# Kernel tuning notes

Measured on AMD Instinct MI355X. Metric: run time of the kernel, lower is better.

## Reference

```python
import jax, jax.numpy as jnp
import numpy as np

NUM_CLASSES = 10
OUT_DIM = 16
NUM_ROUTING = 3
ROUTING_BIAS = 0.1


def _squash(s):
    # s: [B, C, D]; norm over last (out_capsule) dim, matches torch norm(dim=2)
    norm = jnp.linalg.norm(s, axis=2, keepdims=True)
    # s / (1+norm^2) / norm * norm^2 == s * norm / (1 + norm^2)
    return s * norm / (1.0 + norm * norm)


def setup_inputs() -> dict:
    key = jax.random.key(0)
    k1, k2 = jax.random.split(key)
    B, N, IN_DIM = 256, 2304, 8
    x = jax.random.normal(k1, (B, N, IN_DIM), dtype=jnp.float32)
    # kaiming-normal-ish init for W [N, in_dim, classes*out_dim]
    W = jax.random.normal(k2, (N, IN_DIM, NUM_CLASSES * OUT_DIM), dtype=jnp.float32) * np.sqrt(2.0 / IN_DIM)
    return {"x": x, "W": W}


def reference(x, W):
    B, N, _ = x.shape
    # broadcast-multiply+sum in original == per-capsule matmul
    u_hat = jnp.einsum('bni,nio->bno', x, W).reshape(B, N, NUM_CLASSES, OUT_DIM)
    u_hat_sg = jax.lax.stop_gradient(u_hat)
    b = jnp.zeros((B, N, NUM_CLASSES), dtype=x.dtype)
    v = None
    for i in range(NUM_ROUTING):
        c = jax.nn.softmax(b, axis=2)  # [B, N, C]
        if i == NUM_ROUTING - 1:
            s = jnp.einsum('bnc,bncd->bcd', c, u_hat) + ROUTING_BIAS
            v = _squash(s)
        else:
            s = jnp.einsum('bnc,bncd->bcd', c, u_hat_sg) + ROUTING_BIAS
            # NOTE: original updates b with pre-squash s (not v) -- kept faithful
            b = b + jnp.einsum('bncd,bcd->bnc', u_hat_sg, s)
    return v
```

## Files before the change

### kernel.cpp

```cpp
#include <hip/hip_runtime.h>
#include <math.h>

#define B_TOT   256
#define N_TOT   2304
#define IN_DIM  8
#define NC      10
#define OD      16
#define CD      160
#define RBIAS   0.1f

#define BTILE    64
#define NS       192
#define NPB      (N_TOT / NS)
#define NTHREADS 640
#define XR       (NPB * IN_DIM + 4)
#define LB       72
#define NF4      (B_TOT * CD / 4)
#define RCOLS    32
#define RGRPS    8
#define RYPER    (NS / RGRPS)

template <int FIRST>
__global__ __launch_bounds__(NTHREADS) void routing_round(
    const float* __restrict__ x,
    const float* __restrict__ W,
    const float* __restrict__ S_acc,
    float* __restrict__ part)
{
    __shared__ float sh_x[BTILE * XR];
    __shared__ float sh_lg[2][NC * LB];

    const int tid = threadIdx.x;
    const int b0  = blockIdx.x * BTILE;
    const int n0  = blockIdx.y * NPB;
    const int b   = tid & 63;
    const int cu  = __builtin_amdgcn_readfirstlane(tid >> 6);

    {
        const int XT4 = BTILE * (NPB * IN_DIM / 4);
        for (int k = tid; k < XT4; k += NTHREADS) {
            int bb   = k / (NPB * 2);
            int off4 = k - bb * (NPB * 2);
            float4 v = *(const float4*)(x + ((size_t)(b0 + bb) * N_TOT + n0) * IN_DIM + off4 * 4);
            *(float4*)(&sh_x[bb * XR + off4 * 4]) = v;
        }
    }

    float S[OD];
    if (!FIRST) {
        const float4* sp = (const float4*)(S_acc + (size_t)(b0 + b) * CD + cu * OD);
        #pragma unroll
        for (int q = 0; q < 4; q++) ((float4*)S)[q] = sp[q];
    }

    float acc[OD];
    #pragma unroll
    for (int d = 0; d < OD; d++) acc[d] = 0.f;

    __syncthreads();

    const float* Wc = W + cu * OD;

    for (int nn = 0; nn < NPB; nn++) {
        float xf[IN_DIM];
        {
            const float4* xp = (const float4*)(&sh_x[b * XR + nn * IN_DIM]);
            ((float4*)xf)[0] = xp[0];
            ((float4*)xf)[1] = xp[1];
        }

        const float* Wn = Wc + (size_t)(n0 + nn) * (IN_DIM * CD);
        float u[OD];
        #pragma unroll
        for (int d = 0; d < OD; d++) u[d] = xf[0] * Wn[d];
        #pragma unroll
        for (int i = 1; i < IN_DIM; i++) {
            const float* Wi = Wn + i * CD;
            #pragma unroll
            for (int d = 0; d < OD; d++) u[d] = fmaf(xf[i], Wi[d], u[d]);
        }

        if (!FIRST) {
            const int cur = nn & 1;
            float lg = 0.f;
            #pragma unroll
            for (int d = 0; d < OD; d++) lg = fmaf(u[d], S[d], lg);
            sh_lg[cur][cu * LB + b] = lg;
            __syncthreads();

            float m = -1e30f;
            float row[NC];
            #pragma unroll
            for (int k = 0; k < NC; k++) {
                row[k] = sh_lg[cur][k * LB + b];
                m = fmaxf(m, row[k]);
            }
            float den = 0.f;
            #pragma unroll
            for (int k = 0; k < NC; k++) den += __expf(row[k] - m);
            float cw = __expf(lg - m) / den;

            #pragma unroll
            for (int d = 0; d < OD; d++) acc[d] = fmaf(cw, u[d], acc[d]);
        } else {
            #pragma unroll
            for (int d = 0; d < OD; d++) acc[d] += u[d];
        }
    }

    float* dst = part + ((size_t)blockIdx.y * B_TOT + (b0 + b)) * CD + cu * OD;
    #pragma unroll
    for (int q = 0; q < 4; q++)
        ((float4*)dst)[q] = ((float4*)acc)[q];
}

__global__ __launch_bounds__(256) void reduce_round(
    const float* __restrict__ part,
    float* __restrict__ S_acc,
    float* __restrict__ v_out,
    float scale, int round)
{
    __shared__ float4 sh[RGRPS][RCOLS];

    const int col = threadIdx.x & (RCOLS - 1);
    const int grp = threadIdx.x >> 5;
    const int g   = blockIdx.x * RCOLS + col;

    const float4* p4 = (const float4*)part + (size_t)grp * NF4 + g;
    float4 s = { 0.f, 0.f, 0.f, 0.f };
    #pragma unroll 4
    for (int y = 0; y < RYPER; y++) {
        float4 t = p4[(size_t)y * RGRPS * NF4];
        s.x += t.x; s.y += t.y; s.z += t.z; s.w += t.w;
    }
    sh[grp][col] = s;
    __syncthreads();

    if (threadIdx.x < RCOLS) {
        float4 t = { 0.f, 0.f, 0.f, 0.f };
        #pragma unroll
        for (int k = 0; k < RGRPS; k++) {
            float4 q = sh[k][col];
            t.x += q.x; t.y += q.y; t.z += q.z; t.w += q.w;
        }
        t.x = t.x * scale + RBIAS;
        t.y = t.y * scale + RBIAS;
        t.z = t.z * scale + RBIAS;
        t.w = t.w * scale + RBIAS;

        if (round == 0) {
            ((float4*)S_acc)[g] = t;
        } else if (round == 1) {
            float4 o = ((float4*)S_acc)[g];
            o.x += t.x; o.y += t.y; o.z += t.z; o.w += t.w;
            ((float4*)S_acc)[g] = o;
        } else {
            float ss = t.x * t.x + t.y * t.y + t.z * t.z + t.w * t.w;
            ss += __shfl_xor(ss, 1, 64);
            ss += __shfl_xor(ss, 2, 64);
            float norm = sqrtf(ss);
            float k2 = norm / (1.0f + ss);
            float4 v = { t.x * k2, t.y * k2, t.z * k2, t.w * k2 };
            ((float4*)v_out)[g] = v;
        }
    }
}

extern "C" void kernel_launch(void* const* d_in, const int* in_sizes, int n_in,
                              void* d_out, int out_size, void* d_ws, size_t ws_size,
                              hipStream_t stream) {
    const float* x = (const float*)d_in[0];
    const float* W = (const float*)d_in[1];
    float* out = (float*)d_out;

    float* part  = (float*)d_ws;
    float* S_acc = part + (size_t)NS * B_TOT * CD;

    const dim3 rgrid(B_TOT / BTILE, NS);
    const int  RG = NF4 / RCOLS;

    routing_round<1><<<rgrid, NTHREADS, 0, stream>>>(x, W, S_acc, part);
    reduce_round<<<RG, 256, 0, stream>>>(part, S_acc, out, 0.1f, 0);

    routing_round<0><<<rgrid, NTHREADS, 0, stream>>>(x, W, S_acc, part);
    reduce_round<<<RG, 256, 0, stream>>>(part, S_acc, out, 1.0f, 1);

    routing_round<0><<<rgrid, NTHREADS, 0, stream>>>(x, W, S_acc, part);
    reduce_round<<<RG, 256, 0, stream>>>(part, S_acc, out, 1.0f, 2);
}
```

Measured before the change: 214.2 us.

## Compute u_hat with split-bf16 MFMA and shuffle-based softmax routing

```diff
diff --git a/kernel.cpp b/kernel.cpp
--- a/kernel.cpp
+++ b/kernel.cpp
@@ -9,109 +9,135 @@
 #define CD      160
 #define RBIAS   0.1f
 
-#define BTILE    64
-#define NS       192
-#define NPB      (N_TOT / NS)
-#define NTHREADS 640
-#define XR       (NPB * IN_DIM + 4)
-#define LB       72
-#define NF4      (B_TOT * CD / 4)
-#define RCOLS    32
-#define RGRPS    8
-#define RYPER    (NS / RGRPS)
+#define NS      128
+#define NPB     (N_TOT / NS)
+#define WROW    (IN_DIM * CD)
+#define NF4     (B_TOT * CD / 4)
+#define NXCD    8
+
+typedef __attribute__((ext_vector_type(8))) short bf16x8;
+typedef __attribute__((ext_vector_type(4))) float f32x4;
+
+__device__ __forceinline__ unsigned int rne_hi(unsigned int b) {
+    return (b + 0x7FFFu + ((b >> 16) & 1u)) & 0xFFFF0000u;
+}
+__device__ __forceinline__ void split2(float f, unsigned int& h, unsigned int& l) {
+    unsigned int xb = __float_as_uint(f);
+    h = rne_hi(xb);
+    float fl = f - __uint_as_float(h);
+    l = __float_as_uint(fl) & 0xFFFF0000u;
+}
 
 template <int FIRST>
-__global__ __launch_bounds__(NTHREADS) void routing_round(
+__global__ __launch_bounds__(512) void routing_round(
     const float* __restrict__ x,
     const float* __restrict__ W,
     const float* __restrict__ S_acc,
     float* __restrict__ part)
 {
-    __shared__ float sh_x[BTILE * XR];
-    __shared__ float sh_lg[2][NC * LB];
-
-    const int tid = threadIdx.x;
-    const int b0  = blockIdx.x * BTILE;
-    const int n0  = blockIdx.y * NPB;
-    const int b   = tid & 63;
-    const int cu  = __builtin_amdgcn_readfirstlane(tid >> 6);
-
-    {
-        const int XT4 = BTILE * (NPB * IN_DIM / 4);
-        for (int k = tid; k < XT4; k += NTHREADS) {
-            int bb   = k / (NPB * 2);
-            int off4 = k - bb * (NPB * 2);
-            float4 v = *(const float4*)(x + ((size_t)(b0 + bb) * N_TOT + n0) * IN_DIM + off4 * 4);
-            *(float4*)(&sh_x[bb * XR + off4 * 4]) = v;
-        }
-    }
-
-    float S[OD];
+    const int tid  = threadIdx.x;
+    const int lane = tid & 63;
+    const int w    = tid >> 6;
+    const int col  = lane & 15;
+    const int g    = lane >> 4;
+
+    const int bid   = blockIdx.x;
+    const int xcd   = bid & (NXCD - 1);
+    const int slot  = bid >> 3;
+    const int y     = xcd * 16 + (slot & 15);
+    const int bhalf = slot >> 4;
+    const int b0    = bhalf * 128 + w * 16;
+    const int n0    = y * NPB;
+
+    const int brow = b0 + 4 * g;
+
+    f32x4 S[NC];
     if (!FIRST) {
-        const float4* sp = (const float4*)(S_acc + (size_t)(b0 + b) * CD + cu * OD);
-        #pragma unroll
-        for (int q = 0; q < 4; q++) ((float4*)S)[q] = sp[q];
-    }
-
-    float acc[OD];
+        #pragma unroll
+        for (int c = 0; c < NC; c++)
+            #pragma unroll
+            for (int r = 0; r < 4; r++)
+                S[c][r] = S_acc[(size_t)(brow + r) * CD + c * OD + col];
+    }
+
+    f32x4 acc[NC];
     #pragma unroll
-    for (int d = 0; d < OD; d++) acc[d] = 0.f;
-
-    __syncthreads();
-
-    const float* Wc = W + cu * OD;
+    for (int c = 0; c < NC; c++) acc[c] = (f32x4){0.f, 0.f, 0.f, 0.f};
+
+    const float* xp = x + ((size_t)(b0 + col) * N_TOT + n0) * IN_DIM + g;
+    const float* wp = W + (size_t)n0 * WROW + g * CD + col;
 
     for (int nn = 0; nn < NPB; nn++) {
-        float xf[IN_DIM];
-        {
-            const float4* xp = (const float4*)(&sh_x[b * XR + nn * IN_DIM]);
-            ((float4*)xf)[0] = xp[0];
-            ((float4*)xf)[1] = xp[1];
-        }
-
-        const float* Wn = Wc + (size_t)(n0 + nn) * (IN_DIM * CD);
-        float u[OD];
-        #pragma unroll
-        for (int d = 0; d < OD; d++) u[d] = xf[0] * Wn[d];
-        #pragma unroll
-        for (int i = 1; i < IN_DIM; i++) {
-            const float* Wi = Wn + i * CD;
+        const float f0 = xp[0];
+        const float f1 = xp[4];
+        unsigned int h0, l0, h1, l1;
+        split2(f0, h0, l0);
+        split2(f1, h1, l1);
+        union { unsigned int d[4]; bf16x8 v; } A;
+        A.d[0] = (h0 >> 16) | h0;
+        A.d[1] = (l0 >> 16) | l0;
+        A.d[2] = (h1 >> 16) | h1;
+        A.d[3] = (l1 >> 16) | l1;
+
+        f32x4 u[NC];
+        #pragma unroll
+        for (int c = 0; c < NC; c++) {
+            const float wlo = wp[c * OD];
+            const float whi = wp[640 + c * OD];
+            unsigned int wh0, wl0, wh1, wl1;
+            split2(wlo, wh0, wl0);
+            split2(whi, wh1, wl1);
+            union { unsigned int d[4]; bf16x8 v; } Bf;
+            const unsigned int p0 = (wh0 >> 16) | wl0;
+            const unsigned int p1 = (wh1 >> 16) | wl1;
+            Bf.d[0] = p0; Bf.d[1] = p0;
+            Bf.d[2] = p1; Bf.d[3] = p1;
+            u[c] = __builtin_amdgcn_mfma_f32_16x16x32_bf16(
+                       A.v, Bf.v, (f32x4){0.f, 0.f, 0.f, 0.f}, 0, 0, 0);
+        }
+
+        if (!FIRST) {
             #pragma unroll
-            for (int d = 0; d < OD; d++) u[d] = fmaf(xf[i], Wi[d], u[d]);
-        }
-
-        if (!FIRST) {
-            const int cur = nn & 1;
-            float lg = 0.f;
-            #pragma unroll
-            for (int d = 0; d < OD; d++) lg = fmaf(u[d], S[d], lg);
-            sh_lg[cur][cu * LB + b] = lg;
-            __syncthreads();
-
-            float m = -1e30f;
-            float row[NC];
-            #pragma unroll
-            for (int k = 0; k < NC; k++) {
-                row[k] = sh_lg[cur][k * LB + b];
-                m = fmaxf(m, row[k]);
+            for (int r = 0; r < 4; r++) {
+                float lg[NC];
+                #pragma unroll
+                for (int c = 0; c < NC; c++) {
+                    float p = u[c][r] * S[c][r];
+                    p += __shfl_xor(p, 1, 64);
+                    p += __shfl_xor(p, 2, 64);
+                    p += __shfl_xor(p, 4, 64);
+                    p += __shfl_xor(p, 8, 64);
+                    lg[c] = p;
+                }
+                float m = lg[0];
+                #pragma unroll
+                for (int c = 1; c < NC; c++) m = fmaxf(m, lg[c]);
+                float den = 0.f;
+                float e[NC];
+                #pragma unroll
+                for (int c = 0; c < NC; c++) { e[c] = __expf(lg[c] - m); den += e[c]; }
+                const float rden = 1.f / den;
+                #pragma unroll
+                for (int c = 0; c < NC; c++)
+                    acc[c][r] = fmaf(e[c] * rden, u[c][r], acc[c][r]);
             }
-            float den = 0.f;
-            #pragma unroll
-            for (int k = 0; k < NC; k++) den += __expf(row[k] - m);
-            float cw = __expf(lg - m) / den;
-
-            #pragma unroll
-            for (int d = 0; d < OD; d++) acc[d] = fmaf(cw, u[d], acc[d]);
         } else {
             #pragma unroll
-            for (int d = 0; d < OD; d++) acc[d] += u[d];
-        }
-    }
-
-    float* dst = part + ((size_t)blockIdx.y * B_TOT + (b0 + b)) * CD + cu * OD;
+            for (int c = 0; c < NC; c++)
+                #pragma unroll
+                for (int r = 0; r < 4; r++) acc[c][r] += u[c][r];
+        }
+
+        xp += IN_DIM;
+        wp += WROW;
+    }
+
+    float* dst = part + (size_t)y * B_TOT * CD;
     #pragma unroll
-    for (int q = 0; q < 4; q++)
-        ((float4*)dst)[q] = ((float4*)acc)[q];
+    for (int c = 0; c < NC; c++)
+        #pragma unroll
+        for (int r = 0; r < 4; r++)
+            dst[(size_t)(brow + r) * CD + c * OD + col] = acc[c][r];
 }
 
 __global__ __launch_bounds__(256) void reduce_round(
@@ -120,26 +146,26 @@
     float* __restrict__ v_out,
     float scale, int round)
 {
-    __shared__ float4 sh[RGRPS][RCOLS];
-
-    const int col = threadIdx.x & (RCOLS - 1);
-    const int grp = threadIdx.x >> 5;
-    const int g   = blockIdx.x * RCOLS + col;
+    __shared__ float4 sh[4][64];
+
+    const int col = threadIdx.x & 63;
+    const int grp = threadIdx.x >> 6;
+    const int g   = blockIdx.x * 64 + col;
 
     const float4* p4 = (const float4*)part + (size_t)grp * NF4 + g;
     float4 s = { 0.f, 0.f, 0.f, 0.f };
-    #pragma unroll 4
-    for (int y = 0; y < RYPER; y++) {
-        float4 t = p4[(size_t)y * RGRPS * NF4];
+    #pragma unroll 8
+    for (int k = 0; k < NS / 4; k++) {
+        float4 t = p4[(size_t)k * 4 * NF4];
         s.x += t.x; s.y += t.y; s.z += t.z; s.w += t.w;
     }
     sh[grp][col] = s;
     __syncthreads();
 
-    if (threadIdx.x < RCOLS) {
+    if (threadIdx.x < 64) {
         float4 t = { 0.f, 0.f, 0.f, 0.f };
         #pragma unroll
-        for (int k = 0; k < RGRPS; k++) {
+        for (int k = 0; k < 4; k++) {
             float4 q = sh[k][col];
             t.x += q.x; t.y += q.y; t.z += q.z; t.w += q.w;
         }
@@ -176,15 +202,15 @@
     float* part  = (float*)d_ws;
     float* S_acc = part + (size_t)NS * B_TOT * CD;
 
-    const dim3 rgrid(B_TOT / BTILE, NS);
-    const int  RG = NF4 / RCOLS;
-
-    routing_round<1><<<rgrid, NTHREADS, 0, stream>>>(x, W, S_acc, part);
+    const dim3 rgrid(256);
+    const int  RG = NF4 / 64;
+
+    routing_round<1><<<rgrid, 512, 0, stream>>>(x, W, S_acc, part);
     reduce_round<<<RG, 256, 0, stream>>>(part, S_acc, out, 0.1f, 0);
 
-    routing_round<0><<<rgrid, NTHREADS, 0, stream>>>(x, W, S_acc, part);
+    routing_round<0><<<rgrid, 512, 0, stream>>>(x, W, S_acc, part);
     reduce_round<<<RG, 256, 0, stream>>>(part, S_acc, out, 1.0f, 1);
 
-    routing_round<0><<<rgrid, NTHREADS, 0, stream>>>(x, W, S_acc, part);
+    routing_round<0><<<rgrid, 512, 0, stream>>>(x, W, S_acc, part);
     reduce_round<<<RG, 256, 0, stream>>>(part, S_acc, out, 1.0f, 2);
 }
```

Measured after the change: 389.4 us. 81.8% more time.
